# Performance work log

Measured on AMD Instinct MI355X. Metric: run time of the kernel, lower is better.

Reference implementation:

```python
import jax, jax.numpy as jnp
import numpy as np

HIDDEN_DIM = 64
TIER_SPECS = [(4, 64), (8, 32), (16, 16)]
VOCAB_SIZE = 64
B = 131072


def setup_inputs() -> dict:
    key = jax.random.key(0)
    ks = jax.random.split(key, 16)
    inp = {
        "query_h": jax.random.normal(ks[0], (B, HIDDEN_DIM), dtype=jnp.float32),
        "mem0": jax.random.normal(ks[1], (B, 4, 64), dtype=jnp.float32),
        "mem1": jax.random.normal(ks[2], (B, 8, 32), dtype=jnp.float32),
        "mem2": jax.random.normal(ks[3], (B, 16, 16), dtype=jnp.float32),
    }
    # per-tier down-proj (HIDDEN->dim) and up-proj (dim->HIDDEN), torch Linear layout [out,in]
    for i, (_, dim) in enumerate(TIER_SPECS):
        s = 1.0 / np.sqrt(HIDDEN_DIM)
        inp[f"Wp{i}"] = jax.random.uniform(ks[4 + i], (dim, HIDDEN_DIM), minval=-s, maxval=s, dtype=jnp.float32)
        inp[f"bp{i}"] = jax.random.uniform(ks[7 + i], (dim,), minval=-s, maxval=s, dtype=jnp.float32)
        su = 1.0 / np.sqrt(dim)
        inp[f"Wu{i}"] = jax.random.uniform(ks[10 + i], (HIDDEN_DIM, dim), minval=-su, maxval=su, dtype=jnp.float32)
        inp[f"bu{i}"] = jax.random.uniform(ks[13 + i], (HIDDEN_DIM,), minval=-su, maxval=su, dtype=jnp.float32)
    sc = 1.0 / np.sqrt(HIDDEN_DIM)
    inp["Wc"] = jax.random.uniform(jax.random.fold_in(key, 99), (VOCAB_SIZE, HIDDEN_DIM), minval=-sc, maxval=sc, dtype=jnp.float32)
    inp["bc"] = jax.random.uniform(jax.random.fold_in(key, 100), (VOCAB_SIZE,), minval=-sc, maxval=sc, dtype=jnp.float32)
    return inp


def _tier(q, mem, Wp, bp, Wu, bu, dim):
    qp = q @ Wp.T + bp                                   # [B, dim]
    sims = jnp.einsum('bsd,bd->bs', mem, qp) / (dim ** 0.5)  # [B, S]
    w = jax.nn.softmax(sims, axis=-1)
    conf = w.max(axis=-1)                                # [B]
    retrieved = jnp.einsum('bs,bsd->bd', w, mem)         # [B, dim]
    return retrieved @ Wu.T + bu, conf                   # [B, HIDDEN], [B]


def reference(query_h, mem0, mem1, mem2,
              Wp0, bp0, Wp1, bp1, Wp2, bp2,
              Wu0, bu0, Wu1, bu1, Wu2, bu2, Wc, bc):
    mems = [mem0, mem1, mem2]
    Wps, bps = [Wp0, Wp1, Wp2], [bp0, bp1, bp2]
    Wus, bus = [Wu0, Wu1, Wu2], [bu0, bu1, bu2]
    results, confs = [], []
    for i, (_, dim) in enumerate(TIER_SPECS):
        r, c = _tier(query_h, mems[i], Wps[i], bps[i], Wus[i], bus[i], dim)
        results.append(r)
        confs.append(c)
    confs = jax.nn.softmax(jnp.stack(confs, axis=1), axis=-1)  # [B, 3]
    result = sum(confs[:, i:i + 1] * results[i] for i in range(3))
    return result @ Wc.T + bc
```

## Files before the change

### kernel.cpp

```cpp
#include <hip/hip_runtime.h>

#define NROWS 131072
#define GRID1 1024
#define ITERS 8

#define DPP_XOR1 0xB1
#define DPP_XOR2 0x4E
#define DPP_HMIR 0x141
#define DPP_ROR1 0x121
#define DPP_ROR2 0x122
#define DPP_ROR4 0x124
#define DPP_ROR8 0x128

template<int C>
__device__ __forceinline__ float fdpp(float x) {
    return __int_as_float(__builtin_amdgcn_mov_dpp(__float_as_int(x), C, 0xF, 0xF, true));
}

__device__ __forceinline__ float dot4(float4 a, float4 b) {
    return fmaf(a.x, b.x, fmaf(a.y, b.y, fmaf(a.z, b.z, a.w * b.w)));
}

struct Smem {
    float Wp[112 * 68];
    float bpb[112];
    float Waug[64 * 116];
    float qpbuf[4][4][112];
    float rbuf[4][4][116];
};

__device__ __forceinline__ float tier0_proc(int lane, float4 m, const float* qp, float* rb) {
    float4 qv = *reinterpret_cast<const float4*>(qp + 4 * (lane >> 2));
    float p = dot4(m, qv);
    p += fdpp<DPP_ROR4>(p);
    p += fdpp<DPP_ROR8>(p);
    p += __shfl_xor(p, 16, 64);
    p += __shfl_xor(p, 32, 64);
    float mx = fmaxf(p, fdpp<DPP_XOR1>(p));
    mx = fmaxf(mx, fdpp<DPP_XOR2>(mx));
    float e = __expf(p - mx);
    float den = e + fdpp<DPP_XOR1>(e);
    den += fdpp<DPP_XOR2>(den);
    float4 rv = make_float4(m.x * e, m.y * e, m.z * e, m.w * e);
    rv.x += fdpp<DPP_XOR1>(rv.x); rv.y += fdpp<DPP_XOR1>(rv.y);
    rv.z += fdpp<DPP_XOR1>(rv.z); rv.w += fdpp<DPP_XOR1>(rv.w);
    rv.x += fdpp<DPP_XOR2>(rv.x); rv.y += fdpp<DPP_XOR2>(rv.y);
    rv.z += fdpp<DPP_XOR2>(rv.z); rv.w += fdpp<DPP_XOR2>(rv.w);
    if ((lane & 3) == 0) *reinterpret_cast<float4*>(rb + 4 * (lane >> 2)) = rv;
    return den;
}

__device__ __forceinline__ float tier1_proc(int lane, float4 m, const float* qp, float* rb) {
    float4 qv = *reinterpret_cast<const float4*>(qp + 4 * (lane >> 3));
    float p = dot4(m, qv);
    p += fdpp<DPP_ROR8>(p);
    p += __shfl_xor(p, 16, 64);
    p += __shfl_xor(p, 32, 64);
    float mx = fmaxf(p, fdpp<DPP_XOR1>(p));
    mx = fmaxf(mx, fdpp<DPP_XOR2>(mx));
    mx = fmaxf(mx, fdpp<DPP_HMIR>(mx));
    float e = __expf(p - mx);
    float den = e + fdpp<DPP_XOR1>(e);
    den += fdpp<DPP_XOR2>(den);
    den += fdpp<DPP_HMIR>(den);
    float4 rv = make_float4(m.x * e, m.y * e, m.z * e, m.w * e);
    rv.x += fdpp<DPP_XOR1>(rv.x); rv.y += fdpp<DPP_XOR1>(rv.y);
    rv.z += fdpp<DPP_XOR1>(rv.z); rv.w += fdpp<DPP_XOR1>(rv.w);
    rv.x += fdpp<DPP_XOR2>(rv.x); rv.y += fdpp<DPP_XOR2>(rv.y);
    rv.z += fdpp<DPP_XOR2>(rv.z); rv.w += fdpp<DPP_XOR2>(rv.w);
    rv.x += fdpp<DPP_HMIR>(rv.x); rv.y += fdpp<DPP_HMIR>(rv.y);
    rv.z += fdpp<DPP_HMIR>(rv.z); rv.w += fdpp<DPP_HMIR>(rv.w);
    if ((lane & 7) == 0) *reinterpret_cast<float4*>(rb + 4 * (lane >> 3)) = rv;
    return den;
}

__device__ __forceinline__ float tier2_proc(int lane, float4 m, const float* qp, float* rb) {
    float4 qv = *reinterpret_cast<const float4*>(qp + 4 * (lane >> 4));
    float p = dot4(m, qv);
    p += __shfl_xor(p, 16, 64);
    p += __shfl_xor(p, 32, 64);
    float mx = fmaxf(p, fdpp<DPP_ROR1>(p));
    mx = fmaxf(mx, fdpp<DPP_ROR2>(mx));
    mx = fmaxf(mx, fdpp<DPP_ROR4>(mx));
    mx = fmaxf(mx, fdpp<DPP_ROR8>(mx));
    float e = __expf(p - mx);
    float den = e + fdpp<DPP_ROR1>(e);
    den += fdpp<DPP_ROR2>(den);
    den += fdpp<DPP_ROR4>(den);
    den += fdpp<DPP_ROR8>(den);
    float4 rv = make_float4(m.x * e, m.y * e, m.z * e, m.w * e);
    rv.x += fdpp<DPP_ROR1>(rv.x); rv.y += fdpp<DPP_ROR1>(rv.y);
    rv.z += fdpp<DPP_ROR1>(rv.z); rv.w += fdpp<DPP_ROR1>(rv.w);
    rv.x += fdpp<DPP_ROR2>(rv.x); rv.y += fdpp<DPP_ROR2>(rv.y);
    rv.z += fdpp<DPP_ROR2>(rv.z); rv.w += fdpp<DPP_ROR2>(rv.w);
    rv.x += fdpp<DPP_ROR4>(rv.x); rv.y += fdpp<DPP_ROR4>(rv.y);
    rv.z += fdpp<DPP_ROR4>(rv.z); rv.w += fdpp<DPP_ROR4>(rv.w);
    rv.x += fdpp<DPP_ROR8>(rv.x); rv.y += fdpp<DPP_ROR8>(rv.y);
    rv.z += fdpp<DPP_ROR8>(rv.z); rv.w += fdpp<DPP_ROR8>(rv.w);
    if ((lane & 15) == 0) *reinterpret_cast<float4*>(rb + 4 * (lane >> 4)) = rv;
    return den;
}

__global__ __launch_bounds__(128) void prep_kernel(
    const float* __restrict__ Wu0, const float* __restrict__ Wu1, const float* __restrict__ Wu2,
    const float* __restrict__ bu0, const float* __restrict__ bu1, const float* __restrict__ bu2,
    const float* __restrict__ Wc,  const float* __restrict__ bc,  float* __restrict__ waug) {
    int o = blockIdx.x;
    int c = threadIdx.x;
    if (c >= 116) return;
    float acc = 0.0f;
    if (c < 112) {
        const float* wu; int d, dim;
        if (c < 64)      { wu = Wu0; d = c;      dim = 64; }
        else if (c < 96) { wu = Wu1; d = c - 64; dim = 32; }
        else             { wu = Wu2; d = c - 96; dim = 16; }
        for (int h = 0; h < 64; ++h) acc = fmaf(Wc[o * 64 + h], wu[h * dim + d], acc);
    } else if (c < 115) {
        const float* bu = (c == 112) ? bu0 : (c == 113) ? bu1 : bu2;
        for (int h = 0; h < 64; ++h) acc = fmaf(Wc[o * 64 + h], bu[h], acc);
    } else {
        acc = bc[o];
    }
    waug[o * 116 + c] = acc;
}

__global__ __launch_bounds__(256, 2) void retrieval_kernel(
    const float* __restrict__ query,
    const float* __restrict__ mem0, const float* __restrict__ mem1, const float* __restrict__ mem2,
    const float* __restrict__ Wp0, const float* __restrict__ bp0,
    const float* __restrict__ Wp1, const float* __restrict__ bp1,
    const float* __restrict__ Wp2, const float* __restrict__ bp2,
    const float* __restrict__ waug, float* __restrict__ out) {
    __shared__ Smem sm;
    const int t = threadIdx.x;
    const int wv = t >> 6;
    const int lane = t & 63;

    for (int idx = t; idx < 4096; idx += 256) { int r = idx >> 6, k = idx & 63; sm.Wp[r * 68 + k] = Wp0[idx] * 0.125f; }
    for (int idx = t; idx < 2048; idx += 256) { int r = idx >> 6, k = idx & 63; sm.Wp[(64 + r) * 68 + k] = Wp1[idx] * 0.17677669529663687f; }
    for (int idx = t; idx < 1024; idx += 256) { int r = idx >> 6, k = idx & 63; sm.Wp[(96 + r) * 68 + k] = Wp2[idx] * 0.25f; }
    if (t < 112) {
        float sc = (t < 64) ? 0.125f : (t < 96) ? 0.17677669529663687f : 0.25f;
        float v  = (t < 64) ? bp0[t] : (t < 96) ? bp1[t - 64] : bp2[t - 96];
        sm.bpb[t] = v * sc;
    }
    for (int idx = t; idx < 7424; idx += 256) sm.Waug[idx] = waug[idx];
    __syncthreads();

    const float4* w0p = reinterpret_cast<const float4*>(&sm.Wp[lane * 68]);
    const float4* w1p = reinterpret_cast<const float4*>(&sm.Wp[(64 + (lane & 31)) * 68]);
    const float4* w2p = reinterpret_cast<const float4*>(&sm.Wp[(96 + (lane & 15)) * 68]);
    const float4* war = reinterpret_cast<const float4*>(&sm.Waug[lane * 116]);
    const float b0 = sm.bpb[lane];
    const float b1 = sm.bpb[64 + (lane & 31)];
    const float b2 = sm.bpb[96 + (lane & 15)];

    const int mi0 = 16 * (lane & 3)  + (lane >> 2);
    const int mi1 = 8  * (lane & 7)  + (lane >> 3);
    const int mi2 = 4  * (lane & 15) + (lane >> 4);

    const int blockRow0 = blockIdx.x * (ITERS * 16);

    for (int it = 0; it < ITERS; ++it) {
        const int r0 = blockRow0 + it * 16 + wv * 4;

        float4 mpre[3][4];
#pragma unroll
        for (int j = 0; j < 4; ++j) {
            mpre[0][j] = reinterpret_cast<const float4*>(mem0 + (size_t)(r0 + j) * 256)[mi0];
            mpre[1][j] = reinterpret_cast<const float4*>(mem1 + (size_t)(r0 + j) * 256)[mi1];
            mpre[2][j] = reinterpret_cast<const float4*>(mem2 + (size_t)(r0 + j) * 256)[mi2];
        }

        const float4* qg0 = reinterpret_cast<const float4*>(query + (size_t)(r0 + 0) * 64);
        const float4* qg1 = reinterpret_cast<const float4*>(query + (size_t)(r0 + 1) * 64);
        const float4* qg2 = reinterpret_cast<const float4*>(query + (size_t)(r0 + 2) * 64);
        const float4* qg3 = reinterpret_cast<const float4*>(query + (size_t)(r0 + 3) * 64);
        float a0[4], a1[4], a2[4];
#pragma unroll
        for (int j = 0; j < 4; ++j) { a0[j] = b0; a1[j] = b1; a2[j] = b2; }
#pragma unroll 4
        for (int kb = 0; kb < 16; ++kb) {
            float4 w0 = w0p[kb], w1 = w1p[kb], w2 = w2p[kb];
            float4 qv0 = qg0[kb], qv1 = qg1[kb], qv2 = qg2[kb], qv3 = qg3[kb];
            a0[0] = fmaf(w0.x, qv0.x, fmaf(w0.y, qv0.y, fmaf(w0.z, qv0.z, fmaf(w0.w, qv0.w, a0[0]))));
            a1[0] = fmaf(w1.x, qv0.x, fmaf(w1.y, qv0.y, fmaf(w1.z, qv0.z, fmaf(w1.w, qv0.w, a1[0]))));
            a2[0] = fmaf(w2.x, qv0.x, fmaf(w2.y, qv0.y, fmaf(w2.z, qv0.z, fmaf(w2.w, qv0.w, a2[0]))));
            a0[1] = fmaf(w0.x, qv1.x, fmaf(w0.y, qv1.y, fmaf(w0.z, qv1.z, fmaf(w0.w, qv1.w, a0[1]))));
            a1[1] = fmaf(w1.x, qv1.x, fmaf(w1.y, qv1.y, fmaf(w1.z, qv1.z, fmaf(w1.w, qv1.w, a1[1]))));
            a2[1] = fmaf(w2.x, qv1.x, fmaf(w2.y, qv1.y, fmaf(w2.z, qv1.z, fmaf(w2.w, qv1.w, a2[1]))));
            a0[2] = fmaf(w0.x, qv2.x, fmaf(w0.y, qv2.y, fmaf(w0.z, qv2.z, fmaf(w0.w, qv2.w, a0[2]))));
            a1[2] = fmaf(w1.x, qv2.x, fmaf(w1.y, qv2.y, fmaf(w1.z, qv2.z, fmaf(w1.w, qv2.w, a1[2]))));
            a2[2] = fmaf(w2.x, qv2.x, fmaf(w2.y, qv2.y, fmaf(w2.z, qv2.z, fmaf(w2.w, qv2.w, a2[2]))));
            a0[3] = fmaf(w0.x, qv3.x, fmaf(w0.y, qv3.y, fmaf(w0.z, qv3.z, fmaf(w0.w, qv3.w, a0[3]))));
            a1[3] = fmaf(w1.x, qv3.x, fmaf(w1.y, qv3.y, fmaf(w1.z, qv3.z, fmaf(w1.w, qv3.w, a1[3]))));
            a2[3] = fmaf(w2.x, qv3.x, fmaf(w2.y, qv3.y, fmaf(w2.z, qv3.z, fmaf(w2.w, qv3.w, a2[3]))));
        }
#pragma unroll
        for (int j = 0; j < 4; ++j) {
            sm.qpbuf[wv][j][lane] = a0[j];
            if (lane < 32) sm.qpbuf[wv][j][64 + lane] = a1[j];
            if (lane < 16) sm.qpbuf[wv][j][96 + lane] = a2[j];
        }

        float cf0[4], cf1[4], cf2[4];
#pragma unroll
        for (int j = 0; j < 4; ++j) {
            float* qp = &sm.qpbuf[wv][j][0];
            float* rb = &sm.rbuf[wv][j][0];
            float den0 = tier0_proc(lane, mpre[0][j], qp, rb);
            float den1 = tier1_proc(lane, mpre[1][j], qp + 64, rb + 64);
            float den2 = tier2_proc(lane, mpre[2][j], qp + 96, rb + 96);
            float c0 = __frcp_rn(den0), c1 = __frcp_rn(den1), c2 = __frcp_rn(den2);
            float cm = fmaxf(c0, fmaxf(c1, c2));
            float e0 = __expf(c0 - cm), e1 = __expf(c1 - cm), e2 = __expf(c2 - cm);
            float ics = __frcp_rn(e0 + e1 + e2);
            float cw0 = e0 * ics, cw1 = e1 * ics, cw2 = e2 * ics;
            cf0[j] = cw0 * c0;
            cf1[j] = cw1 * c1;
            cf2[j] = cw2 * c2;
            float ext = (lane == 0) ? cw0 : (lane == 1) ? cw1 : (lane == 2) ? cw2 : 1.0f;
            if (lane < 4) rb[112 + lane] = ext;
        }

        float t0[4] = {0, 0, 0, 0}, t1[4] = {0, 0, 0, 0}, t2[4] = {0, 0, 0, 0}, t3[4];
#pragma unroll 4
        for (int cb = 0; cb < 16; ++cb) {
            float4 w = war[cb];
#pragma unroll
            for (int j = 0; j < 4; ++j) {
                float4 rv = reinterpret_cast<const float4*>(&sm.rbuf[wv][j][0])[cb];
                t0[j] = fmaf(w.x, rv.x, fmaf(w.y, rv.y, fmaf(w.z, rv.z, fmaf(w.w, rv.w, t0[j]))));
            }
        }
#pragma unroll 4
        for (int cb = 16; cb < 24; ++cb) {
            float4 w = war[cb];
#pragma unroll
            for (int j = 0; j < 4; ++j) {
                float4 rv = reinterpret_cast<const float4*>(&sm.rbuf[wv][j][0])[cb];
                t1[j] = fmaf(w.x, rv.x, fmaf(w.y, rv.y, fmaf(w.z, rv.z, fmaf(w.w, rv.w, t1[j]))));
            }
        }
#pragma unroll
        for (int cb = 24; cb < 28; ++cb) {
            float4 w = war[cb];
#pragma unroll
            for (int j = 0; j < 4; ++j) {
                float4 rv = reinterpret_cast<const float4*>(&sm.rbuf[wv][j][0])[cb];
                t2[j] = fmaf(w.x, rv.x, fmaf(w.y, rv.y, fmaf(w.z, rv.z, fmaf(w.w, rv.w, t2[j]))));
            }
        }
        {
            float4 w = war[28];
#pragma unroll
            for (int j = 0; j < 4; ++j) {
                float4 rv = reinterpret_cast<const float4*>(&sm.rbuf[wv][j][0])[28];
                t3[j] = dot4(w, rv);
            }
        }
#pragma unroll
        for (int j = 0; j < 4; ++j) {
            out[(r0 + j) * 64 + lane] =
                fmaf(cf0[j], t0[j], fmaf(cf1[j], t1[j], fmaf(cf2[j], t2[j], t3[j])));
        }
    }
}

extern "C" void kernel_launch(void* const* d_in, const int* in_sizes, int n_in,
                              void* d_out, int out_size, void* d_ws, size_t ws_size,
                              hipStream_t stream) {
    const float* query = (const float*)d_in[0];
    const float* mem0  = (const float*)d_in[1];
    const float* mem1  = (const float*)d_in[2];
    const float* mem2  = (const float*)d_in[3];
    const float* Wp0   = (const float*)d_in[4];
    const float* bp0   = (const float*)d_in[5];
    const float* Wu0   = (const float*)d_in[6];
    const float* bu0   = (const float*)d_in[7];
    const float* Wp1   = (const float*)d_in[8];
    const float* bp1   = (const float*)d_in[9];
    const float* Wu1   = (const float*)d_in[10];
    const float* bu1   = (const float*)d_in[11];
    const float* Wp2   = (const float*)d_in[12];
    const float* bp2   = (const float*)d_in[13];
    const float* Wu2   = (const float*)d_in[14];
    const float* bu2   = (const float*)d_in[15];
    const float* Wc    = (const float*)d_in[16];
    const float* bc    = (const float*)d_in[17];
    float* waug = (float*)d_ws;
    float* outp = (float*)d_out;

    prep_kernel<<<64, 128, 0, stream>>>(Wu0, Wu1, Wu2, bu0, bu1, bu2, Wc, bc, waug);
    retrieval_kernel<<<GRID1, 256, 0, stream>>>(query, mem0, mem1, mem2,
                                                Wp0, bp0, Wp1, bp1, Wp2, bp2,
                                                waug, outp);
}
```

Before: 536.8 us.

## Shrink LDS and registers to raise occupancy, use packed FMA and cheaper cross-lane ops

```diff
diff --git a/kernel.cpp b/kernel.cpp
--- a/kernel.cpp
+++ b/kernel.cpp
@@ -1,6 +1,8 @@
 #include <hip/hip_runtime.h>
 
-#define NROWS 131072
+typedef float v2f __attribute__((ext_vector_type(2)));
+typedef float v4f __attribute__((ext_vector_type(4)));
+
 #define GRID1 1024
 #define ITERS 8
 
@@ -16,46 +18,50 @@
 __device__ __forceinline__ float fdpp(float x) {
     return __int_as_float(__builtin_amdgcn_mov_dpp(__float_as_int(x), C, 0xF, 0xF, true));
 }
-
-__device__ __forceinline__ float dot4(float4 a, float4 b) {
+__device__ __forceinline__ float swz16(float x) {
+    return __int_as_float(__builtin_amdgcn_ds_swizzle(__float_as_int(x), 0x401F));
+}
+__device__ __forceinline__ float bperm(int addr, float x) {
+    return __int_as_float(__builtin_amdgcn_ds_bpermute(addr, __float_as_int(x)));
+}
+__device__ __forceinline__ float dot4(v4f a, v4f b) {
     return fmaf(a.x, b.x, fmaf(a.y, b.y, fmaf(a.z, b.z, a.w * b.w)));
+}
+__device__ __forceinline__ v2f pkfma(v2f a, v2f b, v2f c) {
+    return __builtin_elementwise_fma(a, b, c);
 }
 
 struct Smem {
     float Wp[112 * 68];
     float bpb[112];
-    float Waug[64 * 116];
-    float qpbuf[4][4][112];
-    float rbuf[4][4][116];
+    float scratch[4][4][116];
 };
 
-__device__ __forceinline__ float tier0_proc(int lane, float4 m, const float* qp, float* rb) {
-    float4 qv = *reinterpret_cast<const float4*>(qp + 4 * (lane >> 2));
+__device__ __forceinline__ float tier0_proc(int lane, int bp32, v4f m, v4f qv, float* rb) {
     float p = dot4(m, qv);
     p += fdpp<DPP_ROR4>(p);
     p += fdpp<DPP_ROR8>(p);
-    p += __shfl_xor(p, 16, 64);
-    p += __shfl_xor(p, 32, 64);
+    p += swz16(p);
+    p += bperm(bp32, p);
     float mx = fmaxf(p, fdpp<DPP_XOR1>(p));
     mx = fmaxf(mx, fdpp<DPP_XOR2>(mx));
     float e = __expf(p - mx);
     float den = e + fdpp<DPP_XOR1>(e);
     den += fdpp<DPP_XOR2>(den);
-    float4 rv = make_float4(m.x * e, m.y * e, m.z * e, m.w * e);
+    v4f rv = m * e;
     rv.x += fdpp<DPP_XOR1>(rv.x); rv.y += fdpp<DPP_XOR1>(rv.y);
     rv.z += fdpp<DPP_XOR1>(rv.z); rv.w += fdpp<DPP_XOR1>(rv.w);
     rv.x += fdpp<DPP_XOR2>(rv.x); rv.y += fdpp<DPP_XOR2>(rv.y);
     rv.z += fdpp<DPP_XOR2>(rv.z); rv.w += fdpp<DPP_XOR2>(rv.w);
-    if ((lane & 3) == 0) *reinterpret_cast<float4*>(rb + 4 * (lane >> 2)) = rv;
+    if ((lane & 3) == 0) *reinterpret_cast<v4f*>(rb + 4 * (lane >> 2)) = rv;
     return den;
 }
 
-__device__ __forceinline__ float tier1_proc(int lane, float4 m, const float* qp, float* rb) {
-    float4 qv = *reinterpret_cast<const float4*>(qp + 4 * (lane >> 3));
+__device__ __forceinline__ float tier1_proc(int lane, int bp32, v4f m, v4f qv, float* rb) {
     float p = dot4(m, qv);
     p += fdpp<DPP_ROR8>(p);
-    p += __shfl_xor(p, 16, 64);
-    p += __shfl_xor(p, 32, 64);
+    p += swz16(p);
+    p += bperm(bp32, p);
     float mx = fmaxf(p, fdpp<DPP_XOR1>(p));
     mx = fmaxf(mx, fdpp<DPP_XOR2>(mx));
     mx = fmaxf(mx, fdpp<DPP_HMIR>(mx));
@@ -63,22 +69,21 @@
     float den = e + fdpp<DPP_XOR1>(e);
     den += fdpp<DPP_XOR2>(den);
     den += fdpp<DPP_HMIR>(den);
-    float4 rv = make_float4(m.x * e, m.y * e, m.z * e, m.w * e);
+    v4f rv = m * e;
     rv.x += fdpp<DPP_XOR1>(rv.x); rv.y += fdpp<DPP_XOR1>(rv.y);
     rv.z += fdpp<DPP_XOR1>(rv.z); rv.w += fdpp<DPP_XOR1>(rv.w);
     rv.x += fdpp<DPP_XOR2>(rv.x); rv.y += fdpp<DPP_XOR2>(rv.y);
     rv.z += fdpp<DPP_XOR2>(rv.z); rv.w += fdpp<DPP_XOR2>(rv.w);
     rv.x += fdpp<DPP_HMIR>(rv.x); rv.y += fdpp<DPP_HMIR>(rv.y);
     rv.z += fdpp<DPP_HMIR>(rv.z); rv.w += fdpp<DPP_HMIR>(rv.w);
-    if ((lane & 7) == 0) *reinterpret_cast<float4*>(rb + 4 * (lane >> 3)) = rv;
+    if ((lane & 7) == 0) *reinterpret_cast<v4f*>(rb + 4 * (lane >> 3)) = rv;
     return den;
 }
 
-__device__ __forceinline__ float tier2_proc(int lane, float4 m, const float* qp, float* rb) {
-    float4 qv = *reinterpret_cast<const float4*>(qp + 4 * (lane >> 4));
+__device__ __forceinline__ float tier2_proc(int lane, int bp32, v4f m, v4f qv, float* rb) {
     float p = dot4(m, qv);
-    p += __shfl_xor(p, 16, 64);
-    p += __shfl_xor(p, 32, 64);
+    p += swz16(p);
+    p += bperm(bp32, p);
     float mx = fmaxf(p, fdpp<DPP_ROR1>(p));
     mx = fmaxf(mx, fdpp<DPP_ROR2>(mx));
     mx = fmaxf(mx, fdpp<DPP_ROR4>(mx));
@@ -88,7 +93,7 @@
     den += fdpp<DPP_ROR2>(den);
     den += fdpp<DPP_ROR4>(den);
     den += fdpp<DPP_ROR8>(den);
-    float4 rv = make_float4(m.x * e, m.y * e, m.z * e, m.w * e);
+    v4f rv = m * e;
     rv.x += fdpp<DPP_ROR1>(rv.x); rv.y += fdpp<DPP_ROR1>(rv.y);
     rv.z += fdpp<DPP_ROR1>(rv.z); rv.w += fdpp<DPP_ROR1>(rv.w);
     rv.x += fdpp<DPP_ROR2>(rv.x); rv.y += fdpp<DPP_ROR2>(rv.y);
@@ -97,7 +102,7 @@
     rv.z += fdpp<DPP_ROR4>(rv.z); rv.w += fdpp<DPP_ROR4>(rv.w);
     rv.x += fdpp<DPP_ROR8>(rv.x); rv.y += fdpp<DPP_ROR8>(rv.y);
     rv.z += fdpp<DPP_ROR8>(rv.z); rv.w += fdpp<DPP_ROR8>(rv.w);
-    if ((lane & 15) == 0) *reinterpret_cast<float4*>(rb + 4 * (lane >> 4)) = rv;
+    if ((lane & 15) == 0) *reinterpret_cast<v4f*>(rb + 4 * (lane >> 4)) = rv;
     return den;
 }
 
@@ -124,7 +129,7 @@
     waug[o * 116 + c] = acc;
 }
 
-__global__ __launch_bounds__(256, 2) void retrieval_kernel(
+__global__ __launch_bounds__(256, 4) void retrieval_kernel(
     const float* __restrict__ query,
     const float* __restrict__ mem0, const float* __restrict__ mem1, const float* __restrict__ mem2,
     const float* __restrict__ Wp0, const float* __restrict__ bp0,
@@ -144,17 +149,18 @@
         float v  = (t < 64) ? bp0[t] : (t < 96) ? bp1[t - 64] : bp2[t - 96];
         sm.bpb[t] = v * sc;
     }
-    for (int idx = t; idx < 7424; idx += 256) sm.Waug[idx] = waug[idx];
     __syncthreads();
 
-    const float4* w0p = reinterpret_cast<const float4*>(&sm.Wp[lane * 68]);
-    const float4* w1p = reinterpret_cast<const float4*>(&sm.Wp[(64 + (lane & 31)) * 68]);
-    const float4* w2p = reinterpret_cast<const float4*>(&sm.Wp[(96 + (lane & 15)) * 68]);
-    const float4* war = reinterpret_cast<const float4*>(&sm.Waug[lane * 116]);
+    const v4f* w0p = reinterpret_cast<const v4f*>(&sm.Wp[lane * 68]);
+    const v4f* w1p = reinterpret_cast<const v4f*>(&sm.Wp[(64 + (lane & 31)) * 68]);
+    const v4f* w2p = reinterpret_cast<const v4f*>(&sm.Wp[(96 + (lane & 15)) * 68]);
+    const v4f* wgp = reinterpret_cast<const v4f*>(waug + (size_t)lane * 116);
     const float b0 = sm.bpb[lane];
     const float b1 = sm.bpb[64 + (lane & 31)];
     const float b2 = sm.bpb[96 + (lane & 15)];
 
+    const int bp32 = (lane ^ 32) << 2;
+
     const int mi0 = 16 * (lane & 3)  + (lane >> 2);
     const int mi1 = 8  * (lane & 7)  + (lane >> 3);
     const int mi2 = 4  * (lane & 15) + (lane >> 4);
@@ -164,53 +170,58 @@
     for (int it = 0; it < ITERS; ++it) {
         const int r0 = blockRow0 + it * 16 + wv * 4;
 
-        float4 mpre[3][4];
-#pragma unroll
-        for (int j = 0; j < 4; ++j) {
-            mpre[0][j] = reinterpret_cast<const float4*>(mem0 + (size_t)(r0 + j) * 256)[mi0];
-            mpre[1][j] = reinterpret_cast<const float4*>(mem1 + (size_t)(r0 + j) * 256)[mi1];
-            mpre[2][j] = reinterpret_cast<const float4*>(mem2 + (size_t)(r0 + j) * 256)[mi2];
-        }
-
-        const float4* qg0 = reinterpret_cast<const float4*>(query + (size_t)(r0 + 0) * 64);
-        const float4* qg1 = reinterpret_cast<const float4*>(query + (size_t)(r0 + 1) * 64);
-        const float4* qg2 = reinterpret_cast<const float4*>(query + (size_t)(r0 + 2) * 64);
-        const float4* qg3 = reinterpret_cast<const float4*>(query + (size_t)(r0 + 3) * 64);
-        float a0[4], a1[4], a2[4];
-#pragma unroll
-        for (int j = 0; j < 4; ++j) { a0[j] = b0; a1[j] = b1; a2[j] = b2; }
+        const v4f* qg0 = reinterpret_cast<const v4f*>(query + (size_t)(r0 + 0) * 64);
+        const v4f* qg1 = reinterpret_cast<const v4f*>(query + (size_t)(r0 + 1) * 64);
+        const v4f* qg2 = reinterpret_cast<const v4f*>(query + (size_t)(r0 + 2) * 64);
+        const v4f* qg3 = reinterpret_cast<const v4f*>(query + (size_t)(r0 + 3) * 64);
+        v2f acc0[4], acc1[4], acc2[4];
+#pragma unroll
+        for (int j = 0; j < 4; ++j) { acc0[j] = 0.f; acc1[j] = 0.f; acc2[j] = 0.f; }
 #pragma unroll 4
         for (int kb = 0; kb < 16; ++kb) {
-            float4 w0 = w0p[kb], w1 = w1p[kb], w2 = w2p[kb];
-            float4 qv0 = qg0[kb], qv1 = qg1[kb], qv2 = qg2[kb], qv3 = qg3[kb];
-            a0[0] = fmaf(w0.x, qv0.x, fmaf(w0.y, qv0.y, fmaf(w0.z, qv0.z, fmaf(w0.w, qv0.w, a0[0]))));
-            a1[0] = fmaf(w1.x, qv0.x, fmaf(w1.y, qv0.y, fmaf(w1.z, qv0.z, fmaf(w1.w, qv0.w, a1[0]))));
-            a2[0] = fmaf(w2.x, qv0.x, fmaf(w2.y, qv0.y, fmaf(w2.z, qv0.z, fmaf(w2.w, qv0.w, a2[0]))));
-            a0[1] = fmaf(w0.x, qv1.x, fmaf(w0.y, qv1.y, fmaf(w0.z, qv1.z, fmaf(w0.w, qv1.w, a0[1]))));
-            a1[1] = fmaf(w1.x, qv1.x, fmaf(w1.y, qv1.y, fmaf(w1.z, qv1.z, fmaf(w1.w, qv1.w, a1[1]))));
-            a2[1] = fmaf(w2.x, qv1.x, fmaf(w2.y, qv1.y, fmaf(w2.z, qv1.z, fmaf(w2.w, qv1.w, a2[1]))));
-            a0[2] = fmaf(w0.x, qv2.x, fmaf(w0.y, qv2.y, fmaf(w0.z, qv2.z, fmaf(w0.w, qv2.w, a0[2]))));
-            a1[2] = fmaf(w1.x, qv2.x, fmaf(w1.y, qv2.y, fmaf(w1.z, qv2.z, fmaf(w1.w, qv2.w, a1[2]))));
-            a2[2] = fmaf(w2.x, qv2.x, fmaf(w2.y, qv2.y, fmaf(w2.z, qv2.z, fmaf(w2.w, qv2.w, a2[2]))));
-            a0[3] = fmaf(w0.x, qv3.x, fmaf(w0.y, qv3.y, fmaf(w0.z, qv3.z, fmaf(w0.w, qv3.w, a0[3]))));
-            a1[3] = fmaf(w1.x, qv3.x, fmaf(w1.y, qv3.y, fmaf(w1.z, qv3.z, fmaf(w1.w, qv3.w, a1[3]))));
-            a2[3] = fmaf(w2.x, qv3.x, fmaf(w2.y, qv3.y, fmaf(w2.z, qv3.z, fmaf(w2.w, qv3.w, a2[3]))));
+            v4f w0 = w0p[kb], w1 = w1p[kb], w2 = w2p[kb];
+            v4f q0 = qg0[kb], q1 = qg1[kb], q2 = qg2[kb], q3 = qg3[kb];
+            acc0[0] = pkfma(w0.xy, q0.xy, acc0[0]); acc0[0] = pkfma(w0.zw, q0.zw, acc0[0]);
+            acc1[0] = pkfma(w1.xy, q0.xy, acc1[0]); acc1[0] = pkfma(w1.zw, q0.zw, acc1[0]);
+            acc2[0] = pkfma(w2.xy, q0.xy, acc2[0]); acc2[0] = pkfma(w2.zw, q0.zw, acc2[0]);
+            acc0[1] = pkfma(w0.xy, q1.xy, acc0[1]); acc0[1] = pkfma(w0.zw, q1.zw, acc0[1]);
+            acc1[1] = pkfma(w1.xy, q1.xy, acc1[1]); acc1[1] = pkfma(w1.zw, q1.zw, acc1[1]);
+            acc2[1] = pkfma(w2.xy, q1.xy, acc2[1]); acc2[1] = pkfma(w2.zw, q1.zw, acc2[1]);
+            acc0[2] = pkfma(w0.xy, q2.xy, acc0[2]); acc0[2] = pkfma(w0.zw, q2.zw, acc0[2]);
+            acc1[2] = pkfma(w1.xy, q2.xy, acc1[2]); acc1[2] = pkfma(w1.zw, q2.zw, acc1[2]);
+            acc2[2] = pkfma(w2.xy, q2.xy, acc2[2]); acc2[2] = pkfma(w2.zw, q2.zw, acc2[2]);
+            acc0[3] = pkfma(w0.xy, q3.xy, acc0[3]); acc0[3] = pkfma(w0.zw, q3.zw, acc0[3]);
+            acc1[3] = pkfma(w1.xy, q3.xy, acc1[3]); acc1[3] = pkfma(w1.zw, q3.zw, acc1[3]);
+            acc2[3] = pkfma(w2.xy, q3.xy, acc2[3]); acc2[3] = pkfma(w2.zw, q3.zw, acc2[3]);
         }
 #pragma unroll
         for (int j = 0; j < 4; ++j) {
-            sm.qpbuf[wv][j][lane] = a0[j];
-            if (lane < 32) sm.qpbuf[wv][j][64 + lane] = a1[j];
-            if (lane < 16) sm.qpbuf[wv][j][96 + lane] = a2[j];
-        }
-
+            float* sc = &sm.scratch[wv][j][0];
+            sc[lane] = acc0[j].x + acc0[j].y + b0;
+            if (lane < 32) sc[64 + lane] = acc1[j].x + acc1[j].y + b1;
+            if (lane < 16) sc[96 + lane] = acc2[j].x + acc2[j].y + b2;
+        }
+
+        v4f mcur[3];
+        mcur[0] = reinterpret_cast<const v4f*>(mem0 + (size_t)r0 * 256)[mi0];
+        mcur[1] = reinterpret_cast<const v4f*>(mem1 + (size_t)r0 * 256)[mi1];
+        mcur[2] = reinterpret_cast<const v4f*>(mem2 + (size_t)r0 * 256)[mi2];
         float cf0[4], cf1[4], cf2[4];
 #pragma unroll
         for (int j = 0; j < 4; ++j) {
-            float* qp = &sm.qpbuf[wv][j][0];
-            float* rb = &sm.rbuf[wv][j][0];
-            float den0 = tier0_proc(lane, mpre[0][j], qp, rb);
-            float den1 = tier1_proc(lane, mpre[1][j], qp + 64, rb + 64);
-            float den2 = tier2_proc(lane, mpre[2][j], qp + 96, rb + 96);
+            v4f mnext[3];
+            if (j < 3) {
+                mnext[0] = reinterpret_cast<const v4f*>(mem0 + (size_t)(r0 + j + 1) * 256)[mi0];
+                mnext[1] = reinterpret_cast<const v4f*>(mem1 + (size_t)(r0 + j + 1) * 256)[mi1];
+                mnext[2] = reinterpret_cast<const v4f*>(mem2 + (size_t)(r0 + j + 1) * 256)[mi2];
+            }
+            float* sc = &sm.scratch[wv][j][0];
+            v4f qv0 = *reinterpret_cast<const v4f*>(sc + 4 * (lane >> 2));
+            v4f qv1 = *reinterpret_cast<const v4f*>(sc + 64 + 4 * (lane >> 3));
+            v4f qv2 = *reinterpret_cast<const v4f*>(sc + 96 + 4 * (lane >> 4));
+            float den0 = tier0_proc(lane, bp32, mcur[0], qv0, sc);
+            float den1 = tier1_proc(lane, bp32, mcur[1], qv1, sc + 64);
+            float den2 = tier2_proc(lane, bp32, mcur[2], qv2, sc + 96);
             float c0 = __frcp_rn(den0), c1 = __frcp_rn(den1), c2 = __frcp_rn(den2);
             float cm = fmaxf(c0, fmaxf(c1, c2));
             float e0 = __expf(c0 - cm), e1 = __expf(c1 - cm), e2 = __expf(c2 - cm);
@@ -220,49 +231,55 @@
             cf1[j] = cw1 * c1;
             cf2[j] = cw2 * c2;
             float ext = (lane == 0) ? cw0 : (lane == 1) ? cw1 : (lane == 2) ? cw2 : 1.0f;
-            if (lane < 4) rb[112 + lane] = ext;
-        }
-
-        float t0[4] = {0, 0, 0, 0}, t1[4] = {0, 0, 0, 0}, t2[4] = {0, 0, 0, 0}, t3[4];
+            if (lane < 4) sc[112 + lane] = ext;
+            mcur[0] = mnext[0]; mcur[1] = mnext[1]; mcur[2] = mnext[2];
+        }
+
+        v2f t0a[4] = {{0,0},{0,0},{0,0},{0,0}};
+        v2f t1a[4] = {{0,0},{0,0},{0,0},{0,0}};
+        v2f t2a[4] = {{0,0},{0,0},{0,0},{0,0}};
+        float t3[4];
 #pragma unroll 4
         for (int cb = 0; cb < 16; ++cb) {
-            float4 w = war[cb];
+            v4f w = wgp[cb];
 #pragma unroll
             for (int j = 0; j < 4; ++j) {
-                float4 rv = reinterpret_cast<const float4*>(&sm.rbuf[wv][j][0])[cb];
-                t0[j] = fmaf(w.x, rv.x, fmaf(w.y, rv.y, fmaf(w.z, rv.z, fmaf(w.w, rv.w, t0[j]))));
+                v4f rv = reinterpret_cast<const v4f*>(&sm.scratch[wv][j][0])[cb];
+                t0a[j] = pkfma(w.xy, rv.xy, t0a[j]); t0a[j] = pkfma(w.zw, rv.zw, t0a[j]);
             }
         }
 #pragma unroll 4
         for (int cb = 16; cb < 24; ++cb) {
-            float4 w = war[cb];
+            v4f w = wgp[cb];
 #pragma unroll
             for (int j = 0; j < 4; ++j) {
-                float4 rv = reinterpret_cast<const float4*>(&sm.rbuf[wv][j][0])[cb];
-                t1[j] = fmaf(w.x, rv.x, fmaf(w.y, rv.y, fmaf(w.z, rv.z, fmaf(w.w, rv.w, t1[j]))));
+                v4f rv = reinterpret_cast<const v4f*>(&sm.scratch[wv][j][0])[cb];
+                t1a[j] = pkfma(w.xy, rv.xy, t1a[j]); t1a[j] = pkfma(w.zw, rv.zw, t1a[j]);
             }
         }
 #pragma unroll
         for (int cb = 24; cb < 28; ++cb) {
-            float4 w = war[cb];
+            v4f w = wgp[cb];
 #pragma unroll
             for (int j = 0; j < 4; ++j) {
-                float4 rv = reinterpret_cast<const float4*>(&sm.rbuf[wv][j][0])[cb];
-                t2[j] = fmaf(w.x, rv.x, fmaf(w.y, rv.y, fmaf(w.z, rv.z, fmaf(w.w, rv.w, t2[j]))));
+                v4f rv = reinterpret_cast<const v4f*>(&sm.scratch[wv][j][0])[cb];
+                t2a[j] = pkfma(w.xy, rv.xy, t2a[j]); t2a[j] = pkfma(w.zw, rv.zw, t2a[j]);
             }
         }
         {
-            float4 w = war[28];
+            v4f w = wgp[28];
 #pragma unroll
             for (int j = 0; j < 4; ++j) {
-                float4 rv = reinterpret_cast<const float4*>(&sm.rbuf[wv][j][0])[28];
+                v4f rv = reinterpret_cast<const v4f*>(&sm.scratch[wv][j][0])[28];
                 t3[j] = dot4(w, rv);
             }
         }
 #pragma unroll
         for (int j = 0; j < 4; ++j) {
-            out[(r0 + j) * 64 + lane] =
-                fmaf(cf0[j], t0[j], fmaf(cf1[j], t1[j], fmaf(cf2[j], t2[j], t3[j])));
+            float r = fmaf(cf0[j], t0a[j].x + t0a[j].y,
+                      fmaf(cf1[j], t1a[j].x + t1a[j].y,
+                      fmaf(cf2[j], t2a[j].x + t2a[j].y, t3[j])));
+            out[(size_t)(r0 + j) * 64 + lane] = r;
         }
     }
 }
```

Measured after the change: 583.5 us. 8.7% more time.
